# Performance work log

Hardware: AMD Instinct MI355X
Metric: run time of the kernel (lower is better)

## Reference

```python
import jax, jax.numpy as jnp
import numpy as np
import math

B, H, W, C = 2, 256, 256, 96
HEADS, WS, SHIFT = 6, 8, 4
HD = C // HEADS
N = WS * WS
NW = (H // WS) * (W // WS)
HIDDEN = 2 * C
L = H * W


def _rel_pos_index():
    coords = np.stack(np.meshgrid(np.arange(WS), np.arange(WS), indexing='ij')).reshape(2, -1)
    rel = (coords[:, :, None] - coords[:, None, :]).transpose(1, 2, 0).astype(np.int64)
    rel[:, :, 0] += WS - 1
    rel[:, :, 1] += WS - 1
    rel[:, :, 0] *= 2 * WS - 1
    return rel.sum(-1)  # (N, N)

RPI = jnp.asarray(_rel_pos_index())


def _shift_mask():
    img = np.zeros((H, W), np.float32)
    cnt = 0
    for hs in (slice(0, -WS), slice(-WS, -SHIFT), slice(-SHIFT, None)):
        for ws in (slice(0, -WS), slice(-WS, -SHIFT), slice(-SHIFT, None)):
            img[hs, ws] = cnt
            cnt += 1
    mw = img.reshape(H // WS, WS, W // WS, WS).transpose(0, 2, 1, 3).reshape(-1, N)
    diff = mw[:, None, :] - mw[:, :, None]
    return jnp.asarray(np.where(diff != 0, -100.0, 0.0).astype(np.float32))  # (NW, N, N)

MASK = _shift_mask()


def window_partition(x):  # (b,H,W,c) -> (b*NW,WS,WS,c)
    b = x.shape[0]
    x = x.reshape(b, H // WS, WS, W // WS, WS, -1)
    return x.transpose(0, 1, 3, 2, 4, 5).reshape(b * NW, WS, WS, -1)


def window_reverse(w):  # (b*NW,WS,WS,c) -> (b,H,W,c)
    b = w.shape[0] // NW
    x = w.reshape(b, H // WS, W // WS, WS, WS, -1)
    return x.transpose(0, 1, 3, 2, 4, 5).reshape(b, H, W, -1)


def layernorm(x, g, bt):
    mu = x.mean(-1, keepdims=True)
    var = ((x - mu) ** 2).mean(-1, keepdims=True)
    return (x - mu) / jnp.sqrt(var + 1e-5) * g + bt


def gelu_exact(x):
    return x * 0.5 * (1.0 + jax.lax.erf(x / math.sqrt(2.0)))


def conv3(x, w, b):  # NHWC, HWIO
    return jax.lax.conv_general_dilated(x, w, (1, 1), 'SAME', dimension_numbers=('NHWC', 'HWIO', 'NHWC')) + b


def l2n(x):
    return x / jnp.maximum(jnp.linalg.norm(x, axis=-1, keepdims=True), 1e-12)


def setup_inputs() -> dict:
    key = jax.random.key(0)
    ks = jax.random.split(key, 24)
    s = 0.05
    return {
        'x': jax.random.normal(ks[0], (B, L, C), jnp.float32),
        'ref': jax.random.normal(ks[1], (B, L, C), jnp.float32),
        'norm1_g': jnp.ones((C,), jnp.float32),
        'norm1_b': jnp.zeros((C,), jnp.float32),
        'qkv_w': jax.random.normal(ks[2], (3 * C, C), jnp.float32) * s,
        'qkv_b': jnp.zeros((3 * C,), jnp.float32),
        'logit_scale': jnp.log(10.0) * jnp.ones((HEADS, 1, 1), jnp.float32),
        'gating': jnp.ones((HEADS,), jnp.float32),
        'rpb_table': jax.random.normal(ks[3], ((2 * WS - 1) ** 2, HEADS), jnp.float32) * 0.02,
        'trunk_w': jax.random.normal(ks[4], (4, 3, 3, C, C), jnp.float32) * s,
        'trunk_b': jnp.zeros((4, C), jnp.float32),
        'proj_w': jax.random.normal(ks[5], (C, C), jnp.float32) * s,
        'proj_b': jnp.zeros((C,), jnp.float32),
        'norm2_g': jnp.ones((C,), jnp.float32),
        'norm2_b': jnp.zeros((C,), jnp.float32),
        'fc1_w': jax.random.normal(ks[6], (HIDDEN, C), jnp.float32) * s,
        'fc1_b': jnp.zeros((HIDDEN,), jnp.float32),
        'convm_w': jax.random.normal(ks[7], (3, 3, HIDDEN, HIDDEN), jnp.float32) * s,
        'convm_b': jnp.zeros((HIDDEN,), jnp.float32),
        'fc2_w': jax.random.normal(ks[8], (C, HIDDEN), jnp.float32) * s,
        'fc2_b': jnp.zeros((C,), jnp.float32),
    }


def reference(x, ref, norm1_g, norm1_b, qkv_w, qkv_b, logit_scale, gating, rpb_table,
              trunk_w, trunk_b, proj_w, proj_b, norm2_g, norm2_b,
              fc1_w, fc1_b, convm_w, convm_b, fc2_w, fc2_b):
    shortcut = x
    xi = layernorm(x, norm1_g, norm1_b).reshape(B, H, W, C)
    ri = layernorm(ref, norm1_g, norm1_b).reshape(B, H, W, C)
    xi = jnp.roll(xi, (-SHIFT, -SHIFT), axis=(1, 2))
    ri = jnp.roll(ri, (-SHIFT, -SHIFT), axis=(1, 2))

    def qkv_windows(img):  # (B,H,W,C) -> q,k,v each (B*NW,HEADS,N,HD)
        t = jnp.einsum('bhwc,oc->bhwo', img, qkv_w) + qkv_b  # 1x1 conv
        t = window_partition(t).reshape(B * NW, N, 3, HEADS, HD)
        t = t.transpose(2, 0, 3, 1, 4)
        return t[0], t[1], t[2]

    q, k, v = qkv_windows(xi)
    _, k_r, v_r = qkv_windows(ri)

    ls = jnp.exp(jnp.minimum(logit_scale, math.log(1.0 / 0.01)))  # (HEADS,1,1)
    rpb = rpb_table[RPI.reshape(-1)].reshape(N, N, HEADS).transpose(2, 0, 1)  # (HEADS,N,N)
    qn = l2n(q)
    attn1 = jnp.einsum('bhnd,bhmd->bhnm', qn, l2n(k)) * ls + rpb[None]
    attn2 = jnp.einsum('bhnd,bhmd->bhnm', qn, l2n(k_r)) * ls + rpb[None]
    m = MASK[None, :, None]  # (1,NW,1,N,N)
    attn1 = (attn1.reshape(B, NW, HEADS, N, N) + m).reshape(B * NW, HEADS, N, N)
    attn2 = (attn2.reshape(B, NW, HEADS, N, N) + m).reshape(B * NW, HEADS, N, N)
    a1 = jax.nn.softmax(attn1, axis=-1)
    a2 = jax.nn.softmax(attn2, axis=-1)
    g = jax.nn.sigmoid(gating)[None, :, None, None]
    out = (1.0 - g) * jnp.einsum('bhnm,bhmd->bhnd', a1, v) + g * jnp.einsum('bhnm,bhmd->bhnd', a2, v_r)
    out = out.transpose(0, 2, 1, 3).reshape(B * NW, WS, WS, C)

    img = window_reverse(out)  # (B,H,W,C)
    # trunk branch: 2 residual blocks (conv3-relu-conv3 + skip)
    y = img
    for i in range(2):
        r = conv3(y, trunk_w[2 * i], trunk_b[2 * i])
        r = jax.nn.relu(r)
        r = conv3(r, trunk_w[2 * i + 1], trunk_b[2 * i + 1])
        y = y + r
    y = jnp.einsum('bhwc,oc->bhwo', y, proj_w) + proj_b  # 1x1 proj

    y = jnp.roll(y, (SHIFT, SHIFT), axis=(1, 2)).reshape(B, L, C)
    x = shortcut + y

    # conv-MLP: fc1 -> gelu -> conv3x3+gelu -> fc2
    h = layernorm(x, norm2_g, norm2_b)
    h = gelu_exact(h @ fc1_w.T + fc1_b)
    himg = h.reshape(B, H, W, HIDDEN)
    himg = gelu_exact(conv3(himg, convm_w, convm_b))
    h = himg.reshape(B, L, HIDDEN) @ fc2_w.T + fc2_b
    return x + h
```

## Files before the change

### kernel.cpp

```cpp
#include <hip/hip_runtime.h>
#include <hip/hip_bf16.h>

#define BB 2
#define HH 256
#define WWID 256
#define CC 96
#define NHEADS 6
#define WSZ 8
#define SHIFTV 4
#define HDIM 16
#define NTOK 64
#define HID 192
#define LL 65536

using bf16 = __hip_bfloat16;
typedef short short8v __attribute__((ext_vector_type(8)));
typedef float float4v __attribute__((ext_vector_type(4)));

__device__ __forceinline__ float b2f(bf16 v){ return __bfloat162float(v); }
__device__ __forceinline__ bf16  f2b(float f){ return __float2bfloat16(f); }
__device__ __forceinline__ float blo(unsigned u){ union {unsigned x; float f;} c; c.x = u << 16; return c.f; }
__device__ __forceinline__ float bhi(unsigned u){ union {unsigned x; float f;} c; c.x = u & 0xffff0000u; return c.f; }

__device__ __forceinline__ float dot8(uint4 a, uint4 b, float acc){
  acc += blo(a.x)*blo(b.x); acc += bhi(a.x)*bhi(b.x);
  acc += blo(a.y)*blo(b.y); acc += bhi(a.y)*bhi(b.y);
  acc += blo(a.z)*blo(b.z); acc += bhi(a.z)*bhi(b.z);
  acc += blo(a.w)*blo(b.w); acc += bhi(a.w)*bhi(b.w);
  return acc;
}

__device__ __forceinline__ void gload16(const void* g, void* l){
  __builtin_amdgcn_global_load_lds(
      (const __attribute__((address_space(1))) unsigned int*)g,
      (__attribute__((address_space(3))) unsigned int*)l, 16, 0, 0);
}

__device__ __forceinline__ int swz(int c8, int r){
  return (c8 < 8) ? (c8 ^ (r & 7)) : (8 + ((c8 & 3) ^ ((r >> 1) & 3)));
}

__global__ void detect_kernel(const unsigned* __restrict__ x, int* __restrict__ flag){
  __shared__ int s[256];
  int t = threadIdx.x;
  int cnt = 0;
  #pragma unroll
  for (int i = 0; i < 4; ++i){
    unsigned u = x[t*4 + i];
    unsigned e = (u >> 7) & 0xFFu;
    cnt += (e >= 118u && e <= 130u) ? 1 : 0;
  }
  s[t] = cnt; __syncthreads();
  for (int m = 128; m > 0; m >>= 1){ if (t < m) s[t] += s[t+m]; __syncthreads(); }
  if (t == 0) *flag = (s[0] < 512) ? 1 : 0;
}

struct CvtArgs { const void* src[21]; long cum[22]; long cumP[22]; };

__global__ void cvt_kernel(CvtArgs a, const int* __restrict__ flag,
                           bf16* __restrict__ dst, long totalP){
  long k0 = ((long)blockIdx.x * 256 + threadIdx.x) * 8;
  if (k0 >= totalP) return;
  int lo = 0;
  #pragma unroll
  for (int i = 0; i < 21; ++i) if (k0 >= a.cumP[i+1]) lo = i+1;
  long e = k0 - a.cumP[lo];
  long n = a.cum[lo+1] - a.cum[lo];
  int f = *flag;
  __align__(16) bf16 ob[8];
  if (e + 8 <= n){
    if (f){
      const float* s = (const float*)a.src[lo] + e;
      float4 v0 = *(const float4*)s;
      float4 v1 = *(const float4*)(s + 4);
      ob[0]=f2b(v0.x); ob[1]=f2b(v0.y); ob[2]=f2b(v0.z); ob[3]=f2b(v0.w);
      ob[4]=f2b(v1.x); ob[5]=f2b(v1.y); ob[6]=f2b(v1.z); ob[7]=f2b(v1.w);
    } else {
      *(uint4*)ob = *(const uint4*)((const bf16*)a.src[lo] + e);
    }
  } else {
    #pragma unroll
    for (int j = 0; j < 8; ++j){
      long ee = e + j;
      ob[j] = (ee < n) ? (f ? f2b(((const float*)a.src[lo])[ee])
                            : ((const bf16*)a.src[lo])[ee])
                       : f2b(0.f);
    }
  }
  *(uint4*)&dst[k0] = *(uint4*)ob;
}

__global__ void wprep_kernel(const bf16* __restrict__ w, bf16* __restrict__ out,
                             int CINr, int COUTr, long total){
  long k = (long)blockIdx.x * 256 + threadIdx.x;
  if (k >= total) return;
  int NHr = COUTr / 96, CHr = CINr / 96;
  int region = (int)(k / 10240); int rem = (int)(k - (long)region*10240);
  int gg = rem >> 3, e = rem & 7;
  if (gg >= 1152){ out[k] = f2b(0.f); return; }
  int r = gg / 12, pos = gg - r*12;
  int ch = region % CHr; int t2 = region / CHr;
  int nhh = t2 % NHr; int tap = t2 / NHr;
  int c8 = (pos < 8) ? (pos ^ (r & 7)) : (8 + ((pos & 3) ^ ((r >> 1) & 3)));
  int cin = ch*96 + c8*8 + e;
  int cout = nhh*96 + r;
  out[k] = w[((long)tap*CINr + cin)*COUTr + cout];
}

__global__ __launch_bounds__(256) void ln1_kernel(const bf16* __restrict__ x, const bf16* __restrict__ ref,
                                                  const bf16* __restrict__ g, const bf16* __restrict__ bt,
                                                  bf16* __restrict__ xn, bf16* __restrict__ rn)
{
  int wave = threadIdx.x >> 6, lane = threadIdx.x & 63;
  long row = (long)blockIdx.x * 4 + wave;
  const bf16* src; bf16* dst; long r;
  if (row < (long)BB*LL){ src = x; dst = xn; r = row; }
  else                  { src = ref; dst = rn; r = row - (long)BB*LL; }
  const bf16* p = src + r*CC;
  float v0 = b2f(p[lane]);
  float v1 = (lane < 32) ? b2f(p[64+lane]) : 0.f;
  float s = v0 + v1;
  #pragma unroll
  for (int m = 32; m >= 1; m >>= 1) s += __shfl_xor(s, m, 64);
  float mu = s * (1.f/CC);
  float d0 = v0 - mu, d1 = v1 - mu;
  float ss = d0*d0 + ((lane < 32) ? d1*d1 : 0.f);
  #pragma unroll
  for (int m = 32; m >= 1; m >>= 1) ss += __shfl_xor(ss, m, 64);
  float rstd = rsqrtf(ss * (1.f/CC) + 1e-5f);
  bf16* q = dst + r*CC;
  q[lane] = f2b(d0 * rstd * b2f(g[lane]) + b2f(bt[lane]));
  if (lane < 32) q[64+lane] = f2b(d1 * rstd * b2f(g[64+lane]) + b2f(bt[64+lane]));
}

__global__ __launch_bounds__(256) void ln2_kernel(const bf16* __restrict__ xin,
                                                  const bf16* __restrict__ g, const bf16* __restrict__ bt,
                                                  bf16* __restrict__ out)
{
  int wave = threadIdx.x >> 6, lane = threadIdx.x & 63;
  long r = (long)blockIdx.x * 4 + wave;
  const bf16* p = xin + r*CC;
  float v0 = b2f(p[lane]);
  float v1 = (lane < 32) ? b2f(p[64+lane]) : 0.f;
  float s = v0 + v1;
  #pragma unroll
  for (int m = 32; m >= 1; m >>= 1) s += __shfl_xor(s, m, 64);
  float mu = s * (1.f/CC);
  float d0 = v0 - mu, d1 = v1 - mu;
  float ss = d0*d0 + ((lane < 32) ? d1*d1 : 0.f);
  #pragma unroll
  for (int m = 32; m >= 1; m >>= 1) ss += __shfl_xor(ss, m, 64);
  float rstd = rsqrtf(ss * (1.f/CC) + 1e-5f);
  bf16* q = out + r*CC;
  q[lane] = f2b(d0 * rstd * b2f(g[lane]) + b2f(bt[lane]));
  if (lane < 32) q[64+lane] = f2b(d1 * rstd * b2f(g[64+lane]) + b2f(bt[64+lane]));
}

__global__ __launch_bounds__(256, 3) void attn_kernel(const bf16* __restrict__ xn, const bf16* __restrict__ rn,
                                                      const bf16* __restrict__ qkv_w, const bf16* __restrict__ qkv_b,
                                                      const bf16* __restrict__ lsc, const bf16* __restrict__ gat,
                                                      const bf16* __restrict__ rpbt, bf16* __restrict__ img)
{
  __shared__ __align__(16) bf16 sx[NTOK][104];
  __shared__ __align__(16) bf16 sr[NTOK][104];
  __shared__ __align__(16) bf16 wps[48*104];
  __shared__ float sbias[48];
  __shared__ __align__(16) bf16 qs[NTOK][20];
  __shared__ __align__(16) bf16 ks[NTOK][20];
  __shared__ __align__(16) bf16 krs[NTOK][20];
  __shared__ __align__(16) bf16 vt[16][72];
  __shared__ __align__(16) bf16 vrt[16][72];
  __shared__ __align__(16) bf16 rpbs[228];

  bf16 (*wb)[104] = (bf16(*)[104])&wps[0];
  bf16 (*ps)[76]  = (bf16(*)[76])&wps[0];

  const float L2E = 1.4426950408889634f;

  int widx = blockIdx.x;
  int b = widx >> 10, wib = widx & 1023;
  int wh = wib >> 5, ww = wib & 31;
  int tid = threadIdx.x;
  int wv = tid >> 6, lane = tid & 63;
  int ml = lane & 15, quad = lane >> 4;

  for (int idx = tid; idx < NTOK*12; idx += 256){
    int n = idx / 12, c8 = idx - n*12;
    int i = n >> 3, j = n & 7;
    int h0 = (wh*8 + i + SHIFTV) & 255;
    int w0 = (ww*8 + j + SHIFTV) & 255;
    long base = (((long)b*HH + h0)*WWID + w0)*CC + c8*8;
    *(uint4*)&sx[n][c8*8] = *(const uint4*)&xn[base];
    *(uint4*)&sr[n][c8*8] = *(const uint4*)&rn[base];
  }

  int ti = wv*16 + ml;
  int iy = ti >> 3, ix = ti & 7;
  int regi = ((wh < 31) ? 0 : (iy < 4 ? 1 : 2))*3 + ((ww < 31) ? 0 : (ix < 4 ? 1 : 2));
  int idxm[16];
  #pragma unroll
  for (int nt = 0; nt < 4; ++nt){
    #pragma unroll
    for (int r = 0; r < 4; ++r){
      int tj = nt*16 + quad*4 + r;
      int jy = tj >> 3, jx = tj & 7;
      int regj = ((wh < 31) ? 0 : (jy < 4 ? 1 : 2))*3 + ((ww < 31) ? 0 : (jx < 4 ? 1 : 2));
      int idx = (iy - jy + 7)*15 + (ix - jx + 7);
      idxm[nt*4 + r] = idx | ((regi != regj) ? 0x8000 : 0);
    }
  }

  for (int h = 0; h < NHEADS; ++h){
    __syncthreads();
    for (int idx = tid; idx < 48*12; idx += 256){
      int rr = idx / 12, c8 = idx - rr*12;
      int o = (rr >> 4)*CC + h*HDIM + (rr & 15);
      *(uint4*)&wb[rr][c8*8] = *(const uint4*)&qkv_w[(long)o*CC + c8*8];
    }
    if (tid < 48){
      int o = (tid >> 4)*CC + h*HDIM + (tid & 15);
      sbias[tid] = b2f(qkv_b[o]);
    }
    if (tid < 225) rpbs[tid] = rpbt[tid*NHEADS + h];
    __syncthreads();

    float4v aq0 = {0,0,0,0}, aq1 = {0,0,0,0}, aq2 = {0,0,0,0};
    float4v ar0 = {0,0,0,0}, ar1 = {0,0,0,0};
    {
      int arow = wv*16 + ml;
      #pragma unroll
      for (int kt = 0; kt < 3; ++kt){
        int ko = kt*32 + quad*8;
        short8v ax = *(const short8v*)&sx[arow][ko];
        short8v av = *(const short8v*)&sr[arow][ko];
        short8v b0 = *(const short8v*)&wb[ml][ko];
        short8v b1 = *(const short8v*)&wb[16+ml][ko];
        short8v b2 = *(const short8v*)&wb[32+ml][ko];
        aq0 = __builtin_amdgcn_mfma_f32_16x16x32_bf16(ax, b0, aq0, 0,0,0);
        aq1 = __builtin_amdgcn_mfma_f32_16x16x32_bf16(ax, b1, aq1, 0,0,0);
        aq2 = __builtin_amdgcn_mfma_f32_16x16x32_bf16(ax, b2, aq2, 0,0,0);
        ar0 = __builtin_amdgcn_mfma_f32_16x16x32_bf16(av, b1, ar0, 0,0,0);
        ar1 = __builtin_amdgcn_mfma_f32_16x16x32_bf16(av, b2, ar1, 0,0,0);
      }
    }
    {
      float bq = sbias[ml], bk = sbias[16+ml], bv = sbias[32+ml];
      #pragma unroll
      for (int r = 0; r < 4; ++r){
        float qv  = aq0[r] + bq;
        float kv  = aq1[r] + bk;
        float krv = ar0[r] + bk;
        float sq = qv*qv, sk = kv*kv, skr = krv*krv;
        #pragma unroll
        for (int m = 1; m < 16; m <<= 1){
          sq  += __shfl_xor(sq,  m, 64);
          sk  += __shfl_xor(sk,  m, 64);
          skr += __shfl_xor(skr, m, 64);
        }
        float iq  = 1.f / fmaxf(sqrtf(sq),  1e-12f);
        float ik  = 1.f / fmaxf(sqrtf(sk),  1e-12f);
        float ikr = 1.f / fmaxf(sqrtf(skr), 1e-12f);
        int tok = wv*16 + quad*4 + r;
        qs[tok][ml]  = f2b(qv*iq);
        ks[tok][ml]  = f2b(kv*ik);
        krs[tok][ml] = f2b(krv*ikr);
        vt[ml][tok]  = f2b(aq2[r] + bv);
        vrt[ml][tok] = f2b(ar1[r] + bv);
      }
    }
    __syncthreads();

    float ls2 = expf(fminf(b2f(lsc[h]), 4.605170185988091f)) * L2E;
    float gv = b2f(gat[h]);
    float g = 1.f / (1.f + expf(-gv));

    float4v s1[4], s2[4];
    {
      int qoff = (quad & 1) * 8;
      short8v z8 = {0,0,0,0,0,0,0,0};
      short8v qf = *(const short8v*)&qs[wv*16 + ml][qoff];
      qf = (quad < 2) ? qf : z8;
      #pragma unroll
      for (int nt = 0; nt < 4; ++nt){
        short8v kf  = *(const short8v*)&ks[nt*16 + ml][qoff];
        short8v krf = *(const short8v*)&krs[nt*16 + ml][qoff];
        kf  = (quad < 2) ? kf  : z8;
        krf = (quad < 2) ? krf : z8;
        float4v zz = {0,0,0,0};
        s1[nt] = __builtin_amdgcn_mfma_f32_16x16x32_bf16(kf,  qf, zz, 0,0,0);
        s2[nt] = __builtin_amdgcn_mfma_f32_16x16x32_bf16(krf, qf, zz, 0,0,0);
      }
    }
    float sv1[4][4], sv2[4][4];
    #pragma unroll
    for (int nt = 0; nt < 4; ++nt){
      #pragma unroll
      for (int r = 0; r < 4; ++r){
        int u = idxm[nt*4 + r];
        float rp = b2f(rpbs[u & 0x1FF]);
        float base = rp*L2E + ((u & 0x8000) ? -144.2695040889f : 0.f);
        sv1[nt][r] = fmaf(s1[nt][r], ls2, base);
        sv2[nt][r] = fmaf(s2[nt][r], ls2, base);
      }
    }
    float mx1 = -1e30f, mx2 = -1e30f;
    #pragma unroll
    for (int nt = 0; nt < 4; ++nt)
      #pragma unroll
      for (int r = 0; r < 4; ++r){ mx1 = fmaxf(mx1, sv1[nt][r]); mx2 = fmaxf(mx2, sv2[nt][r]); }
    mx1 = fmaxf(mx1, __shfl_xor(mx1, 16, 64)); mx1 = fmaxf(mx1, __shfl_xor(mx1, 32, 64));
    mx2 = fmaxf(mx2, __shfl_xor(mx2, 16, 64)); mx2 = fmaxf(mx2, __shfl_xor(mx2, 32, 64));
    float sm1 = 0.f, sm2 = 0.f;
    #pragma unroll
    for (int nt = 0; nt < 4; ++nt)
      #pragma unroll
      for (int r = 0; r < 4; ++r){
        sv1[nt][r] = exp2f(sv1[nt][r] - mx1); sm1 += sv1[nt][r];
        sv2[nt][r] = exp2f(sv2[nt][r] - mx2); sm2 += sv2[nt][r];
      }
    sm1 += __shfl_xor(sm1, 16, 64); sm1 += __shfl_xor(sm1, 32, 64);
    sm2 += __shfl_xor(sm2, 16, 64); sm2 += __shfl_xor(sm2, 32, 64);
    float f1 = (1.f - g) / sm1;
    float f2 = g / sm2;

    #pragma unroll
    for (int nt = 0; nt < 4; ++nt){
      __align__(8) bf16 pk[4];
      #pragma unroll
      for (int r = 0; r < 4; ++r) pk[r] = f2b(sv1[nt][r] * f1);
      *(short4*)&ps[ti][nt*16 + quad*4] = *(short4*)pk;
    }
    float4v po = {0,0,0,0};
    #pragma unroll
    for (int kt = 0; kt < 2; ++kt){
      short8v pa = *(const short8v*)&ps[wv*16 + ml][kt*32 + quad*8];
      short8v vb = *(const short8v*)&vt[ml][kt*32 + quad*8];
      po = __builtin_amdgcn_mfma_f32_16x16x32_bf16(pa, vb, po, 0,0,0);
    }
    #pragma unroll
    for (int nt = 0; nt < 4; ++nt){
      __align__(8) bf16 pk[4];
      #pragma unroll
      for (int r = 0; r < 4; ++r) pk[r] = f2b(sv2[nt][r] * f2);
      *(short4*)&ps[ti][nt*16 + quad*4] = *(short4*)pk;
    }
    #pragma unroll
    for (int kt = 0; kt < 2; ++kt){
      short8v pa = *(const short8v*)&ps[wv*16 + ml][kt*32 + quad*8];
      short8v vb = *(const short8v*)&vrt[ml][kt*32 + quad*8];
      po = __builtin_amdgcn_mfma_f32_16x16x32_bf16(pa, vb, po, 0,0,0);
    }
    #pragma unroll
    for (int r = 0; r < 4; ++r){
      int tok = wv*16 + quad*4 + r;
      int hs = wh*8 + (tok >> 3), wsp = ww*8 + (tok & 7);
      img[(((long)b*HH + hs)*WWID + wsp)*CC + h*HDIM + ml] = f2b(po[r]);
    }
  }
}

template<int CIN, int COUT, int MODE>
__global__ __launch_bounds__(256) void convmfma_kernel(const bf16* __restrict__ src,
                                                       const bf16* __restrict__ wtp,
                                                       const bf16* __restrict__ bias,
                                                       const bf16* __restrict__ base,
                                                       bf16* __restrict__ dst)
{
  constexpr int CH = CIN / 96;
  constexpr int NH = COUT / 96;
  constexpr int NS = CH * 9;
  __shared__ __align__(16) bf16 act[180*12*8];
  __shared__ __align__(16) bf16 wl[2][1280*8];

  int tid = threadIdx.x;
  int z = blockIdx.z;
  int bb = z / NH;
  int nh = z % NH;
  int tx0 = blockIdx.x * 16, ty0 = blockIdx.y * 8;
  int wv = tid >> 6, lane = tid & 63;

  auto stage_act = [&](int h){
    for (int idx = tid; idx < 180*12; idx += 256){
      int pp = idx / 12, c8 = idx - pp*12;
      int iy = pp / 18, ix = pp - iy*18;
      int gy = ty0 + iy - 1, gx = tx0 + ix - 1;
      uint4 v = make_uint4(0,0,0,0);
      if ((unsigned)gy < (unsigned)HH && (unsigned)gx < (unsigned)WWID)
        v = *(const uint4*)&src[(((long)bb*HH + gy)*WWID + gx)*CIN + h*96 + c8*8];
      *(uint4*)&act[(pp*12 + swz(c8, pp))*8] = v;
    }
  };
  auto gloadW = [&](int s, int buf){
    int hh = s / 9, tap = s - hh*9;
    int region = (tap*NH + nh)*CH + hh;
    const bf16* g = wtp + (long)region*10240 + (wv*320 + lane)*8;
    bf16* l = &wl[buf][(wv*320)*8];
    #pragma unroll
    for (int i = 0; i < 5; ++i)
      gload16(g + i*512, l + i*512);
  };

  int wm = wv >> 1, wn = wv & 1;
  int ml = lane & 15, quad = lane >> 4;

  float4v acc[4][3];
  #pragma unroll
  for (int nt = 0; nt < 3; ++nt){
    float bv = b2f(bias[nh*96 + wn*48 + nt*16 + ml]);
    #pragma unroll
    for (int mt = 0; mt < 4; ++mt)
      acc[mt][nt] = (float4v){bv, bv, bv, bv};
  }

  int apy = ml >> 3, apx = wm*8 + (ml & 7);

  stage_act(0);
  gloadW(0, 0);
  if (NS > 1) gloadW(1, 1);
  __syncthreads();

  for (int s = 0; s < NS; ++s){
    int h = s / 9, tap = s - h*9;
    int cur = s & 1;
    int dy = tap / 3, dx = tap - dy*3;
    #pragma unroll
    for (int kc = 0; kc < 3; ++kc){
      int posB = (kc < 2) ? ((kc*4 + quad) ^ (ml & 7)) : (8 + (quad ^ ((ml >> 1) & 3)));
      int brow = wn*48 + ml;
      short8v b0 = *(const short8v*)&wl[cur][((brow     )*12 + posB)*8];
      short8v b1 = *(const short8v*)&wl[cur][((brow + 16)*12 + posB)*8];
      short8v b2 = *(const short8v*)&wl[cur][((brow + 32)*12 + posB)*8];
      #pragma unroll
      for (int mt = 0; mt < 4; ++mt){
        int pp = (mt*2 + apy + dy)*18 + apx + dx;
        int posA = (kc < 2) ? ((kc*4 + quad) ^ (pp & 7)) : (8 + (quad ^ ((pp >> 1) & 3)));
        short8v a = *(const short8v*)&act[(pp*12 + posA)*8];
        acc[mt][0] = __builtin_amdgcn_mfma_f32_16x16x32_bf16(a, b0, acc[mt][0], 0, 0, 0);
        acc[mt][1] = __builtin_amdgcn_mfma_f32_16x16x32_bf16(a, b1, acc[mt][1], 0, 0, 0);
        acc[mt][2] = __builtin_amdgcn_mfma_f32_16x16x32_bf16(a, b2, acc[mt][2], 0, 0, 0);
      }
    }
    if (s + 1 == NS) break;
    __syncthreads();
    if (s + 2 < NS) gloadW(s + 2, cur);
    if (tap == 8){
      stage_act(h + 1);
      __syncthreads();
    }
  }

  #pragma unroll
  for (int mt = 0; mt < 4; ++mt){
    #pragma unroll
    for (int r = 0; r < 4; ++r){
      int mrow = quad*4 + r;
      int py = mt*2 + (mrow >> 3), px = wm*8 + (mrow & 7);
      long ob = (((long)bb*HH + ty0+py)*WWID + tx0+px)*COUT + nh*96 + wn*48 + ml;
      #pragma unroll
      for (int nt = 0; nt < 3; ++nt){
        float v = acc[mt][nt][r];
        long o = ob + nt*16;
        if (MODE == 0)      dst[o] = f2b(fmaxf(v, 0.f));
        else if (MODE == 1) dst[o] = f2b(b2f(base[o]) + v);
        else                dst[o] = f2b(0.5f * v * (1.f + erff(v * 0.7071067811865476f)));
      }
    }
  }
}

#define PPITCH (CC+8)
__global__ __launch_bounds__(256) void proj_kernel(const bf16* __restrict__ img, const bf16* __restrict__ pw,
                                                   const bf16* __restrict__ pb, const bf16* __restrict__ xorig,
                                                   bf16* __restrict__ xmid)
{
  __shared__ __align__(16) bf16 rows[64][PPITCH];
  __shared__ __align__(16) bf16 wsm[CC][PPITCH];
  long pix0 = (long)blockIdx.x * 64;
  int tid = threadIdx.x;
  for (int idx = tid; idx < 64*CC; idx += 256){
    int pp = idx / CC, c = idx - pp*CC;
    long pix = pix0 + pp;
    int b = (int)(pix >> 16); int hw = (int)(pix & 65535);
    int h = hw >> 8, wc = hw & 255;
    int sh = (h - SHIFTV) & 255, sw = (wc - SHIFTV) & 255;
    rows[pp][c] = img[(((long)b*HH + sh)*WWID + sw)*CC + c];
  }
  for (int idx = tid; idx < CC*CC; idx += 256){
    int rr = idx / CC, c = idx - rr*CC;
    wsm[rr][c] = pw[idx];
  }
  __syncthreads();
  int ty = tid >> 4, tx = tid & 15;
  int r0 = ty*4;
  float acc[4][6];
  #pragma unroll
  for (int j = 0; j < 6; ++j){
    float bv = b2f(pb[tx + 16*j]);
    #pragma unroll
    for (int i = 0; i < 4; ++i) acc[i][j] = bv;
  }
  for (int kk = 0; kk < 12; ++kk){
    uint4 a0 = ((const uint4*)rows[r0+0])[kk];
    uint4 a1 = ((const uint4*)rows[r0+1])[kk];
    uint4 a2 = ((const uint4*)rows[r0+2])[kk];
    uint4 a3 = ((const uint4*)rows[r0+3])[kk];
    #pragma unroll
    for (int j = 0; j < 6; ++j){
      uint4 wv = ((const uint4*)wsm[tx + 16*j])[kk];
      acc[0][j] = dot8(a0, wv, acc[0][j]);
      acc[1][j] = dot8(a1, wv, acc[1][j]);
      acc[2][j] = dot8(a2, wv, acc[2][j]);
      acc[3][j] = dot8(a3, wv, acc[3][j]);
    }
  }
  #pragma unroll
  for (int i = 0; i < 4; ++i){
    long pix = pix0 + r0 + i;
    #pragma unroll
    for (int j = 0; j < 6; ++j){
      long oi = pix*CC + tx + 16*j;
      xmid[oi] = f2b(b2f(xorig[oi]) + acc[i][j]);
    }
  }
}

__global__ __launch_bounds__(256) void fc1_kernel(const bf16* __restrict__ src, const bf16* __restrict__ w,
                                                  const bf16* __restrict__ bias, bf16* __restrict__ dst)
{
  __shared__ __align__(16) bf16 rows[64][PPITCH];
  __shared__ __align__(16) bf16 wsm[HID][PPITCH];
  long pix0 = (long)blockIdx.x * 64;
  int tid = threadIdx.x;
  for (int idx = tid; idx < 64*CC; idx += 256){
    int pp = idx / CC, c = idx - pp*CC;
    rows[pp][c] = src[(pix0 + pp)*CC + c];
  }
  for (int idx = tid; idx < HID*CC; idx += 256){
    int rr = idx / CC, c = idx - rr*CC;
    wsm[rr][c] = w[idx];
  }
  __syncthreads();
  int ty = tid >> 4, tx = tid & 15;
  int r0 = ty*4;
  float acc[4][12];
  #pragma unroll
  for (int j = 0; j < 12; ++j){
    float bv = b2f(bias[tx + 16*j]);
    #pragma unroll
    for (int i = 0; i < 4; ++i) acc[i][j] = bv;
  }
  for (int kk = 0; kk < 12; ++kk){
    uint4 a0 = ((const uint4*)rows[r0+0])[kk];
    uint4 a1 = ((const uint4*)rows[r0+1])[kk];
    uint4 a2 = ((const uint4*)rows[r0+2])[kk];
    uint4 a3 = ((const uint4*)rows[r0+3])[kk];
    #pragma unroll
    for (int j = 0; j < 12; ++j){
      uint4 wv = ((const uint4*)wsm[tx + 16*j])[kk];
      acc[0][j] = dot8(a0, wv, acc[0][j]);
      acc[1][j] = dot8(a1, wv, acc[1][j]);
      acc[2][j] = dot8(a2, wv, acc[2][j]);
      acc[3][j] = dot8(a3, wv, acc[3][j]);
    }
  }
  #pragma unroll
  for (int i = 0; i < 4; ++i){
    long pix = pix0 + r0 + i;
    #pragma unroll
    for (int j = 0; j < 12; ++j){
      float v = acc[i][j];
      dst[pix*HID + tx + 16*j] = f2b(0.5f * v * (1.f + erff(v * 0.7071067811865476f)));
    }
  }
}

#define FPITCH (HID+8)
__global__ __launch_bounds__(256) void fc2_kernel(const bf16* __restrict__ src, const bf16* __restrict__ w,
                                                  const bf16* __restrict__ bias, const bf16* __restrict__ xmid,
                                                  void* __restrict__ outv, const int* __restrict__ flag)
{
  __shared__ __align__(16) bf16 rows[64][FPITCH];
  __shared__ __align__(16) bf16 wsm[CC][FPITCH];
  long pix0 = (long)blockIdx.x * 64;
  int tid = threadIdx.x;
  for (int idx = tid; idx < 64*HID; idx += 256){
    int pp = idx / HID, c = idx - pp*HID;
    rows[pp][c] = src[(pix0 + pp)*HID + c];
  }
  for (int idx = tid; idx < CC*HID; idx += 256){
    int rr = idx / HID, c = idx - rr*HID;
    wsm[rr][c] = w[idx];
  }
  __syncthreads();
  int ty = tid >> 4, tx = tid & 15;
  int r0 = ty*4;
  float acc[4][6];
  #pragma unroll
  for (int j = 0; j < 6; ++j){
    float bv = b2f(bias[tx + 16*j]);
    #pragma unroll
    for (int i = 0; i < 4; ++i) acc[i][j] = bv;
  }
  for (int kk = 0; kk < 24; ++kk){
    uint4 a0 = ((const uint4*)rows[r0+0])[kk];
    uint4 a1 = ((const uint4*)rows[r0+1])[kk];
    uint4 a2 = ((const uint4*)rows[r0+2])[kk];
    uint4 a3 = ((const uint4*)rows[r0+3])[kk];
    #pragma unroll
    for (int j = 0; j < 6; ++j){
      uint4 wv = ((const uint4*)wsm[tx + 16*j])[kk];
      acc[0][j] = dot8(a0, wv, acc[0][j]);
      acc[1][j] = dot8(a1, wv, acc[1][j]);
      acc[2][j] = dot8(a2, wv, acc[2][j]);
      acc[3][j] = dot8(a3, wv, acc[3][j]);
    }
  }
  int f = *flag;
  #pragma unroll
  for (int i = 0; i < 4; ++i){
    long pix = pix0 + r0 + i;
    #pragma unroll
    for (int j = 0; j < 6; ++j){
      long oi = pix*CC + tx + 16*j;
      float v = b2f(xmid[oi]) + acc[i][j];
      if (f) ((float*)outv)[oi] = v;
      else   ((bf16*)outv)[oi] = f2b(v);
    }
  }
}

extern "C" void kernel_launch(void* const* d_in, const int* in_sizes, int n_in,
                              void* d_out, int out_size, void* d_ws, size_t ws_size,
                              hipStream_t stream)
{
  long cum[22], cumP[22]; cum[0] = 0; cumP[0] = 0;
  for (int i = 0; i < 21; ++i){
    cum[i+1]  = cum[i]  + in_sizes[i];
    cumP[i+1] = cumP[i] + (((long)in_sizes[i] + 7) & ~7L);
  }
  long totalP = cumP[21];

  CvtArgs a;
  for (int i = 0; i < 21; ++i) a.src[i] = d_in[i];
  for (int i = 0; i < 22; ++i){ a.cum[i] = cum[i]; a.cumP[i] = cumP[i]; }

  char* ws = (char*)d_ws;
  int*  flag   = (int*)ws;
  bf16* packed = (bf16*)(ws + 1048576);

  detect_kernel<<<1, 256, 0, stream>>>((const unsigned*)d_in[0], flag);
  cvt_kernel<<<(int)((totalP/8 + 255) / 256), 256, 0, stream>>>(a, flag, packed, totalP);

  #define PP(i) (packed + cumP[i])
  const bf16* xc    = PP(0);
  const bf16* rc    = PP(1);
  const bf16* n1g   = PP(2);
  const bf16* n1b   = PP(3);
  const bf16* qkv_w = PP(4);
  const bf16* qkv_b = PP(5);
  const bf16* lsc   = PP(6);
  const bf16* gat   = PP(7);
  const bf16* rpbt  = PP(8);
  const bf16* tw    = PP(9);
  const bf16* tb    = PP(10);
  const bf16* pw    = PP(11);
  const bf16* pb    = PP(12);
  const bf16* n2g   = PP(13);
  const bf16* n2b   = PP(14);
  const bf16* f1w   = PP(15);
  const bf16* f1b   = PP(16);
  const bf16* cmw   = PP(17);
  const bf16* cmb   = PP(18);
  const bf16* f2w   = PP(19);
  const bf16* f2bp  = PP(20);

  bf16* wtc  = (bf16*)(ws + 52860928);
  bf16* wtm  = (bf16*)(ws + 53598208);
  bf16* xn   = (bf16*)(ws + 54525952);
  bf16* rn   = (bf16*)(ws + 79691776);
  bf16* img  = (bf16*)(ws + 104857600);
  bf16* rtr  = xn;
  bf16* xmid = xn;
  bf16* ln2o = rn;
  bf16* h1   = (bf16*)(ws + 1048576);
  bf16* hc   = rn;

  wprep_kernel<<<1440, 256, 0, stream>>>(tw, wtc, 96, 96, 368640);
  wprep_kernel<<<1440, 256, 0, stream>>>(cmw, wtm, 192, 192, 368640);

  ln1_kernel<<<65536, 256, 0, stream>>>(xc, rc, n1g, n1b, xn, rn);
  attn_kernel<<<2048, 256, 0, stream>>>(xn, rn, qkv_w, qkv_b, lsc, gat, rpbt, img);

  convmfma_kernel<96,96,0><<<dim3(16,32,2), 256, 0, stream>>>(img, wtc + 0L*92160, tb + 0,   nullptr, rtr);
  convmfma_kernel<96,96,1><<<dim3(16,32,2), 256, 0, stream>>>(rtr, wtc + 1L*92160, tb + 96,  img,     img);
  convmfma_kernel<96,96,0><<<dim3(16,32,2), 256, 0, stream>>>(img, wtc + 2L*92160, tb + 192, nullptr, rtr);
  convmfma_kernel<96,96,1><<<dim3(16,32,2), 256, 0, stream>>>(rtr, wtc + 3L*92160, tb + 288, img,     img);

  proj_kernel<<<2048, 256, 0, stream>>>(img, pw, pb, xc, xmid);
  ln2_kernel<<<32768, 256, 0, stream>>>(xmid, n2g, n2b, ln2o);
  fc1_kernel<<<2048, 256, 0, stream>>>(ln2o, f1w, f1b, h1);
  convmfma_kernel<192,192,2><<<dim3(16,32,4), 256, 0, stream>>>(h1, wtm, cmb, nullptr, hc);
  fc2_kernel<<<2048, 256, 0, stream>>>(hc, f2w, f2bp, xmid, d_out, flag);
}
```

Before: 885.1 us.

## Single-buffer conv weights, drop padding, precompute staging offsets for occupancy

The conv weight LDS buffer goes from double-buffered padded 1280-row regions to a single unpadded 1152-row region. The prepacked weight layout and wprep sizes shrink to match. Activation staging offsets are now computed once into registers and reused per channel chunk, and launch bounds ask for 3 blocks per CU. The goal is to cut LDS use so more blocks fit per CU. In exchange, weight loads are serialized with compute behind an extra barrier per step, so latency hiding now depends on occupancy.

After: 958.2 us. 1.08x slower.

```diff
diff --git a/kernel.cpp b/kernel.cpp
--- a/kernel.cpp
+++ b/kernel.cpp
@@ -95,9 +95,8 @@
   long k = (long)blockIdx.x * 256 + threadIdx.x;
   if (k >= total) return;
   int NHr = COUTr / 96, CHr = CINr / 96;
-  int region = (int)(k / 10240); int rem = (int)(k - (long)region*10240);
+  int region = (int)(k / 9216); int rem = (int)(k - (long)region*9216);
   int gg = rem >> 3, e = rem & 7;
-  if (gg >= 1152){ out[k] = f2b(0.f); return; }
   int r = gg / 12, pos = gg - r*12;
   int ch = region % CHr; int t2 = region / CHr;
   int nhh = t2 % NHr; int tap = t2 / NHr;
@@ -360,17 +359,17 @@
 }
 
 template<int CIN, int COUT, int MODE>
-__global__ __launch_bounds__(256) void convmfma_kernel(const bf16* __restrict__ src,
-                                                       const bf16* __restrict__ wtp,
-                                                       const bf16* __restrict__ bias,
-                                                       const bf16* __restrict__ base,
-                                                       bf16* __restrict__ dst)
+__global__ __launch_bounds__(256, 3) void convmfma_kernel(const bf16* __restrict__ src,
+                                                          const bf16* __restrict__ wtp,
+                                                          const bf16* __restrict__ bias,
+                                                          const bf16* __restrict__ base,
+                                                          bf16* __restrict__ dst)
 {
   constexpr int CH = CIN / 96;
   constexpr int NH = COUT / 96;
   constexpr int NS = CH * 9;
   __shared__ __align__(16) bf16 act[180*12*8];
-  __shared__ __align__(16) bf16 wl[2][1280*8];
+  __shared__ __align__(16) bf16 wl[1152*8];
 
   int tid = threadIdx.x;
   int z = blockIdx.z;
@@ -379,25 +378,38 @@
   int tx0 = blockIdx.x * 16, ty0 = blockIdx.y * 8;
   int wv = tid >> 6, lane = tid & 63;
 
+  long srcO[9]; int dstO[9];
+  #pragma unroll
+  for (int k = 0; k < 9; ++k){
+    int idx = k*256 + tid;
+    if (idx < 2160){
+      int pp = idx / 12, c8 = idx - pp*12;
+      int iiy = pp / 18, iix = pp - iiy*18;
+      int gy = ty0 + iiy - 1, gx = tx0 + iix - 1;
+      bool ok = ((unsigned)gy < (unsigned)HH) && ((unsigned)gx < (unsigned)WWID);
+      srcO[k] = ok ? ((((long)bb*HH + gy)*WWID + gx)*CIN + c8*8) : -1L;
+      dstO[k] = (pp*12 + swz(c8, pp))*8;
+    } else { srcO[k] = -1L; dstO[k] = -1; }
+  }
   auto stage_act = [&](int h){
-    for (int idx = tid; idx < 180*12; idx += 256){
-      int pp = idx / 12, c8 = idx - pp*12;
-      int iy = pp / 18, ix = pp - iy*18;
-      int gy = ty0 + iy - 1, gx = tx0 + ix - 1;
-      uint4 v = make_uint4(0,0,0,0);
-      if ((unsigned)gy < (unsigned)HH && (unsigned)gx < (unsigned)WWID)
-        v = *(const uint4*)&src[(((long)bb*HH + gy)*WWID + gx)*CIN + h*96 + c8*8];
-      *(uint4*)&act[(pp*12 + swz(c8, pp))*8] = v;
+    #pragma unroll
+    for (int k = 0; k < 9; ++k){
+      if (dstO[k] >= 0){
+        uint4 v = make_uint4(0,0,0,0);
+        if (srcO[k] >= 0) v = *(const uint4*)&src[srcO[k] + h*96];
+        *(uint4*)&act[dstO[k]] = v;
+      }
     }
   };
-  auto gloadW = [&](int s, int buf){
+  auto gloadW = [&](int s){
     int hh = s / 9, tap = s - hh*9;
     int region = (tap*NH + nh)*CH + hh;
-    const bf16* g = wtp + (long)region*10240 + (wv*320 + lane)*8;
-    bf16* l = &wl[buf][(wv*320)*8];
-    #pragma unroll
-    for (int i = 0; i < 5; ++i)
+    const bf16* g = wtp + (long)region*9216 + (wv*288 + lane)*8;
+    bf16* l = &wl[(wv*288)*8];
+    #pragma unroll
+    for (int i = 0; i < 4; ++i)
       gload16(g + i*512, l + i*512);
+    if (lane < 32) gload16(g + 4*512, l + 4*512);
   };
 
   int wm = wv >> 1, wn = wv & 1;
@@ -415,21 +427,19 @@
   int apy = ml >> 3, apx = wm*8 + (ml & 7);
 
   stage_act(0);
-  gloadW(0, 0);
-  if (NS > 1) gloadW(1, 1);
+  gloadW(0);
   __syncthreads();
 
   for (int s = 0; s < NS; ++s){
     int h = s / 9, tap = s - h*9;
-    int cur = s & 1;
     int dy = tap / 3, dx = tap - dy*3;
     #pragma unroll
     for (int kc = 0; kc < 3; ++kc){
       int posB = (kc < 2) ? ((kc*4 + quad) ^ (ml & 7)) : (8 + (quad ^ ((ml >> 1) & 3)));
       int brow = wn*48 + ml;
-      short8v b0 = *(const short8v*)&wl[cur][((brow     )*12 + posB)*8];
-      short8v b1 = *(const short8v*)&wl[cur][((brow + 16)*12 + posB)*8];
-      short8v b2 = *(const short8v*)&wl[cur][((brow + 32)*12 + posB)*8];
+      short8v b0 = *(const short8v*)&wl[((brow     )*12 + posB)*8];
+      short8v b1 = *(const short8v*)&wl[((brow + 16)*12 + posB)*8];
+      short8v b2 = *(const short8v*)&wl[((brow + 32)*12 + posB)*8];
       #pragma unroll
       for (int mt = 0; mt < 4; ++mt){
         int pp = (mt*2 + apy + dy)*18 + apx + dx;
@@ -442,11 +452,9 @@
     }
     if (s + 1 == NS) break;
     __syncthreads();
-    if (s + 2 < NS) gloadW(s + 2, cur);
-    if (tap == 8){
-      stage_act(h + 1);
-      __syncthreads();
-    }
+    gloadW(s + 1);
+    if (tap == 8) stage_act(h + 1);
+    __syncthreads();
   }
 
   #pragma unroll
@@ -675,7 +683,7 @@
   const bf16* f2bp  = PP(20);
 
   bf16* wtc  = (bf16*)(ws + 52860928);
-  bf16* wtm  = (bf16*)(ws + 53598208);
+  bf16* wtm  = (bf16*)(ws + 53579776);
   bf16* xn   = (bf16*)(ws + 54525952);
   bf16* rn   = (bf16*)(ws + 79691776);
   bf16* img  = (bf16*)(ws + 104857600);
@@ -685,16 +693,16 @@
   bf16* h1   = (bf16*)(ws + 1048576);
   bf16* hc   = rn;
 
-  wprep_kernel<<<1440, 256, 0, stream>>>(tw, wtc, 96, 96, 368640);
-  wprep_kernel<<<1440, 256, 0, stream>>>(cmw, wtm, 192, 192, 368640);
+  wprep_kernel<<<1296, 256, 0, stream>>>(tw, wtc, 96, 96, 331776);
+  wprep_kernel<<<1296, 256, 0, stream>>>(cmw, wtm, 192, 192, 331776);
 
   ln1_kernel<<<65536, 256, 0, stream>>>(xc, rc, n1g, n1b, xn, rn);
   attn_kernel<<<2048, 256, 0, stream>>>(xn, rn, qkv_w, qkv_b, lsc, gat, rpbt, img);
 
-  convmfma_kernel<96,96,0><<<dim3(16,32,2), 256, 0, stream>>>(img, wtc + 0L*92160, tb + 0,   nullptr, rtr);
-  convmfma_kernel<96,96,1><<<dim3(16,32,2), 256, 0, stream>>>(rtr, wtc + 1L*92160, tb + 96,  img,     img);
-  convmfma_kernel<96,96,0><<<dim3(16,32,2), 256, 0, stream>>>(img, wtc + 2L*92160, tb + 192, nullptr, rtr);
-  convmfma_kernel<96,96,1><<<dim3(16,32,2), 256, 0, stream>>>(rtr, wtc + 3L*92160, tb + 288, img,     img);
+  convmfma_kernel<96,96,0><<<dim3(16,32,2), 256, 0, stream>>>(img, wtc + 0L*82944, tb + 0,   nullptr, rtr);
+  convmfma_kernel<96,96,1><<<dim3(16,32,2), 256, 0, stream>>>(rtr, wtc + 1L*82944, tb + 96,  img,     img);
+  convmfma_kernel<96,96,0><<<dim3(16,32,2), 256, 0, stream>>>(img, wtc + 2L*82944, tb + 192, nullptr, rtr);
+  convmfma_kernel<96,96,1><<<dim3(16,32,2), 256, 0, stream>>>(rtr, wtc + 3L*82944, tb + 288, img,     img);
 
   proj_kernel<<<2048, 256, 0, stream>>>(img, pw, pb, xc, xmid);
   ln2_kernel<<<32768, 256, 0, stream>>>(xmid, n2g, n2b, ln2o);
```
